# Optimization experiments

Measured on AMD Instinct MI355X. Metric: run time of the kernel, lower is better.

The kernel has to match this reference:

```python
import jax, jax.numpy as jnp
import numpy as np

B = 8; A = 9; NUM_CLASSES = 80
BRANCH_HW = [(80, 80), (40, 40)]; STRIDES = [8, 16]
IMG_H, IMG_W = 640, 640
CLASS_OFFSETS = [0, 0]
SCORE_THR = 0.05; NMS_THR = 0.5; MARGIN = 0.0
PRE_NMS = 1000; POST_NMS = 300
MIN_H, MIN_W = 0.0, 0.0
BBOX_CLIP = float(np.log(1000.0 / 16.0))  # torchvision-style dw/dh clamp


def _make_anchors(H, W, stride):
    # A square anchors per cell, grid-aligned (x1,y1,x2,y2)
    sizes = np.array([16., 32., 64., 20., 40., 80., 24., 48., 96.])[:A]
    cx = (np.arange(W) + 0.5) * stride
    cy = (np.arange(H) + 0.5) * stride
    cy_g, cx_g = np.meshgrid(cy, cx, indexing='ij')  # [H,W]
    half = sizes / 2.0  # [A]
    x1 = cx_g[..., None] - half; y1 = cy_g[..., None] - half
    x2 = cx_g[..., None] + half; y2 = cy_g[..., None] + half
    anc = np.stack([x1, y1, x2, y2], -1).astype(np.float32)  # [H,W,A,4]
    anc = anc.reshape(H, W, A * 4).transpose(2, 0, 1)  # [A*4,H,W]
    return jnp.asarray(np.broadcast_to(anc[None], (B,) + anc.shape).copy())


def setup_inputs() -> dict:
    key = jax.random.key(0)
    ks = jax.random.split(key, 2)
    out = {}
    for i, (Hh, Ww) in enumerate(BRANCH_HW):
        d = jax.random.normal(ks[i], (B, Hh, Ww, A, 4 + NUM_CLASSES), jnp.float32)
        d = d.at[..., :4].multiply(0.25)  # keep box deltas in a sane range
        out['data%d' % i] = d.reshape(B, Hh, Ww, A * (4 + NUM_CLASSES)).transpose(0, 3, 1, 2)
        out['anchors%d' % i] = _make_anchors(Hh, Ww, STRIDES[i])
    return out


def _unfold(t, d):
    b = t.shape[0]
    return jnp.transpose(t, (0, 2, 3, 1)).reshape(b, -1, d)


def _decode(deltas, anchors):
    # BoxCoder((1,1,1,1)).decode_single
    aw = anchors[..., 2] - anchors[..., 0]; ah = anchors[..., 3] - anchors[..., 1]
    acx = anchors[..., 0] + 0.5 * aw; acy = anchors[..., 1] + 0.5 * ah
    dx, dy, dw, dh = (deltas[..., 0], deltas[..., 1], deltas[..., 2], deltas[..., 3])
    pcx = dx * aw + acx; pcy = dy * ah + acy
    pw = jnp.exp(jnp.minimum(dw, BBOX_CLIP)) * aw
    ph = jnp.exp(jnp.minimum(dh, BBOX_CLIP)) * ah
    return jnp.stack([pcx - 0.5 * pw, pcy - 0.5 * ph, pcx + 0.5 * pw, pcy + 0.5 * ph], -1)


def _iou(b):
    area = (b[:, 2] - b[:, 0]) * (b[:, 3] - b[:, 1])
    lt = jnp.maximum(b[:, None, :2], b[None, :, :2])
    rb = jnp.minimum(b[:, None, 2:], b[None, :, 2:])
    wh = jnp.clip(rb - lt, 0.0)
    inter = wh[..., 0] * wh[..., 1]
    return inter / (area[:, None] + area[None, :] - inter + 1e-9)


def _nms_single(boxes, cls, scores):
    # sort by score, take pre_nms_top_k
    sc, idx = jax.lax.top_k(scores, PRE_NMS)
    b = boxes[idx]; c = cls[idx]
    # score threshold + min-hw validity filter (masked instead of dynamic slice)
    valid = (sc >= SCORE_THR) & (b[:, 0] < b[:, 2] - MIN_W) & (b[:, 1] < b[:, 3] - MIN_H)
    iou = _iou(b)  # [PRE,PRE]
    rng = jnp.arange(PRE_NMS)

    def body(i, keep):
        # box j suppressed by kept box i if IoU>thr and score_i - score_j > margin
        sup = keep[i] & (iou[i] > NMS_THR) & ((sc[i] - sc) > MARGIN) & (rng > i)
        return keep & (~sup)

    keep = jax.lax.fori_loop(0, PRE_NMS, body, valid)
    # kept boxes first (score order preserved), then pad_zero to POST_NMS
    order = jnp.argsort(jnp.where(keep, rng, rng + PRE_NMS))[:POST_NMS]
    km = keep[order]
    return (jnp.where(km[:, None], b[order], 0.0),
            jnp.where(km, sc[order], 0.0),
            jnp.where(km, c[order], 0.0))


def reference(data0, data1, anchors0, anchors1):
    datas = [data0, data1]; ancs = [anchors0, anchors1]
    fa, deltas, scores, offs = [], [], [], []
    for i in range(2):
        fa.append(_unfold(ancs[i], 4))
        u = _unfold(datas[i], 4 + NUM_CLASSES)
        deltas.append(u[..., :4]); scores.append(u[..., 4:])
        offs.append(jnp.full((1, u.shape[1]), float(CLASS_OFFSETS[i]), jnp.float32))
    fa = jnp.concatenate(fa, 1); deltas = jnp.concatenate(deltas, 1)
    scores = jnp.concatenate(scores, 1); offs = jnp.concatenate(offs, 1)
    max_sc = scores.max(-1)
    cls = jnp.argmax(scores, -1).astype(jnp.float32) + offs
    boxes = _decode(deltas, fa)
    # clip to image
    x = jnp.clip(boxes[..., 0::2], 0.0, float(IMG_W))
    y = jnp.clip(boxes[..., 1::2], 0.0, float(IMG_H))
    boxes = jnp.stack([x[..., 0], y[..., 0], x[..., 1], y[..., 1]], -1)
    return jax.vmap(_nms_single)(boxes, cls, max_sc)  # ([B,POST,4],[B,POST],[B,POST])
```

## Files before the change

### kernel.cpp

```cpp
#include <hip/hip_runtime.h>
#include <math.h>

#pragma clang fp contract(off)

#define BB      8
#define AA      9
#define NCLS    80
#define NTOT    72000
#define PRE     1000
#define POST    300
#define CAP     4096
#define BCLIP   4.135166556742356f
#define NBLK0   1440
#define NBLK1   360
#define DS1BASE 1843200

__device__ __constant__ float c_sizes[9] = {16.f,32.f,64.f,20.f,40.f,80.f,24.f,48.f,96.f};

__device__ inline unsigned fkey(float s) {
    unsigned u = __float_as_uint(s);
    return (u & 0x80000000u) ? ~u : (u | 0x80000000u);
}
__device__ inline float unfkey(unsigned u) {
    return __uint_as_float((u & 0x80000000u) ? (u ^ 0x80000000u) : ~u);
}

template<int BR>
__device__ inline void stream_impl(int bx, const float* __restrict__ data,
                                   unsigned long long* __restrict__ partial,
                                   float* __restrict__ dstage,
                                   unsigned long long* lkey)
{
    constexpr int ROWF4 = BR ? 400 : 1600;
    int slab, cg, hwq;
    if (BR == 0) { slab = bx / 20; int r = bx % 20; cg = r / 4; hwq = r % 4; }
    else         { slab = bx / 5;  cg = bx % 5;  hwq = 0; }
    int b = slab / 9, a = slab - (slab / 9) * 9;
    int nch = cg ? 16 : 20;
    int c_first = cg ? (4 + cg * 16) : 0;

    for (int i = threadIdx.x; i < 1600; i += 256) lkey[i] = 0ULL;
    __syncthreads();

    const float4* d4 = (const float4*)data;
    size_t rowbase = (size_t)(b * 756 + a * 84 + c_first) * ROWF4 + hwq * 400;
    float4* ds4 = (float4*)dstage;

    int tid = threadIdx.x;
    int rr2 = tid + 256;
    bool s2 = (rr2 < 400);

    for (int c0 = 0; c0 < nch; c0 += 4) {
        float4 v[8];
        #pragma unroll
        for (int u = 0; u < 4; u++) {
            size_t base = rowbase + (size_t)(c0 + u) * ROWF4;
            v[2 * u]     = d4[base + tid];
            v[2 * u + 1] = s2 ? d4[base + rr2] : make_float4(0.f, 0.f, 0.f, 0.f);
        }
        #pragma unroll
        for (int u = 0; u < 4; u++) {
            int ch = c_first + c0 + u;
            if (ch < 4) {
                size_t di0, di1;
                if (BR) { di0 = (size_t)(DS1BASE / 4) + (size_t)(slab * 4 + ch) * 400 + tid;
                          di1 = di0 + 256; }
                else    { di0 = (size_t)(slab * 4 + ch) * 1600 + hwq * 400 + tid;
                          di1 = di0 + 256; }
                ds4[di0] = v[2 * u];
                if (s2) ds4[di1] = v[2 * u + 1];
            } else {
                unsigned icls = ~(unsigned)(ch - 4);
                float4 x = v[2 * u];
                int cell = tid * 4;
                atomicMax(&lkey[cell + 0], ((unsigned long long)fkey(x.x) << 32) | icls);
                atomicMax(&lkey[cell + 1], ((unsigned long long)fkey(x.y) << 32) | icls);
                atomicMax(&lkey[cell + 2], ((unsigned long long)fkey(x.z) << 32) | icls);
                atomicMax(&lkey[cell + 3], ((unsigned long long)fkey(x.w) << 32) | icls);
                if (s2) {
                    float4 y = v[2 * u + 1];
                    int cell2 = rr2 * 4;
                    atomicMax(&lkey[cell2 + 0], ((unsigned long long)fkey(y.x) << 32) | icls);
                    atomicMax(&lkey[cell2 + 1], ((unsigned long long)fkey(y.y) << 32) | icls);
                    atomicMax(&lkey[cell2 + 2], ((unsigned long long)fkey(y.z) << 32) | icls);
                    atomicMax(&lkey[cell2 + 3], ((unsigned long long)fkey(y.w) << 32) | icls);
                }
            }
        }
    }
    __syncthreads();

    size_t pbase = (size_t)cg * 576000 + (size_t)b * 72000
                 + (BR ? (size_t)(57600 + a * 1600) : (size_t)(a * 6400 + hwq * 1600));
    for (int cell = threadIdx.x; cell < 1600; cell += 256)
        partial[pbase + cell] = lkey[cell];
}

__global__ __launch_bounds__(256) void k_stream(
    const float* __restrict__ data0, const float* __restrict__ data1,
    unsigned long long* __restrict__ partial, float* __restrict__ dstage)
{
    __shared__ unsigned long long lkey[1600];
    int bx = blockIdx.x;
    if (bx < NBLK0) stream_impl<0>(bx, data0, partial, dstage, lkey);
    else            stream_impl<1>(bx - NBLK0, data1, partial, dstage, lkey);
}

__global__ __launch_bounds__(256) void k_cells(
    const unsigned long long* __restrict__ partial, const float* __restrict__ dstage,
    float* __restrict__ boxes, float* __restrict__ scores, float* __restrict__ cls,
    unsigned* __restrict__ chist)
{
    __shared__ unsigned lh[256];
    int tid = threadIdx.x;
    lh[tid] = 0;
    __syncthreads();

    int b = blockIdx.y;
    int mm = blockIdx.x * 256 + tid;
    if (mm < 36000) {
        const ulonglong2* p2 = (const ulonglong2*)partial;
        ulonglong2 best = p2[(size_t)b * 36000 + mm];
        #pragma unroll
        for (int g = 1; g < 5; g++) {
            ulonglong2 v = p2[(size_t)g * 288000 + (size_t)b * 36000 + mm];
            if (v.x > best.x) best.x = v.x;
            if (v.y > best.y) best.y = v.y;
        }
        unsigned long long kk[2] = { best.x, best.y };

        int m0 = mm * 2;
        int a, hw, W, STRIDE;
        size_t dbase;
        if (m0 < 57600) {
            a = m0 / 6400; hw = m0 - a * 6400; W = 80; STRIDE = 8;
            dbase = (size_t)((b * 9 + a) * 4) * 6400 + hw;
        } else {
            int m1 = m0 - 57600;
            a = m1 / 1600; hw = m1 - a * 1600; W = 40; STRIDE = 16;
            dbase = (size_t)DS1BASE + (size_t)((b * 9 + a) * 4) * 1600 + hw;
        }
        size_t cstride = (m0 < 57600) ? 6400 : 1600;
        float2 dx = *(const float2*)(dstage + dbase);
        float2 dy = *(const float2*)(dstage + dbase + cstride);
        float2 dw = *(const float2*)(dstage + dbase + 2 * cstride);
        float2 dh = *(const float2*)(dstage + dbase + 3 * cstride);
        float dxa[2] = {dx.x, dx.y}, dya[2] = {dy.x, dy.y};
        float dwa[2] = {dw.x, dw.y}, dha[2] = {dh.x, dh.y};

        float sz = c_sizes[a];
        size_t o = (size_t)b * NTOT + m0;

        #pragma unroll
        for (int k = 0; k < 2; k++) {
            int hwk = hw + k;
            int h = hwk / W;
            int w = hwk - h * W;
            float cy = (h + 0.5f) * (float)STRIDE;
            float cx = (w + 0.5f) * (float)STRIDE;
            float pcx = dxa[k] * sz + cx;
            float pcy = dya[k] * sz + cy;
            float pw  = expf(fminf(dwa[k], BCLIP)) * sz;
            float ph  = expf(fminf(dha[k], BCLIP)) * sz;
            float x1 = fminf(fmaxf(pcx - 0.5f * pw, 0.f), 640.f);
            float y1 = fminf(fmaxf(pcy - 0.5f * ph, 0.f), 640.f);
            float x2 = fminf(fmaxf(pcx + 0.5f * pw, 0.f), 640.f);
            float y2 = fminf(fmaxf(pcy + 0.5f * ph, 0.f), 640.f);
            ((float4*)boxes)[o + k] = make_float4(x1, y1, x2, y2);
            scores[o + k] = unfkey((unsigned)(kk[k] >> 32));
            cls[o + k]    = (float)(~(unsigned)kk[k]);
            atomicAdd(&lh[(unsigned)(kk[k] >> 56)], 1u);
        }
    }
    __syncthreads();
    if (lh[tid]) atomicAdd(&chist[b * 256 + tid], lh[tid]);
}

__global__ __launch_bounds__(256) void k_cscan(const unsigned* __restrict__ chist,
                                               unsigned* __restrict__ Cca)
{
    __shared__ unsigned S[256];
    int b = blockIdx.x, tid = threadIdx.x;
    S[tid] = chist[b * 256 + tid];
    __syncthreads();
    for (int off = 1; off < 256; off <<= 1) {
        unsigned v = S[tid] + ((tid + off < 256) ? S[tid + off] : 0u);
        __syncthreads();
        S[tid] = v;
        __syncthreads();
    }
    if (S[tid] >= (unsigned)PRE && (tid == 255 || S[tid + 1] < (unsigned)PRE)) {
        Cca[b * 2]     = (unsigned)tid;
        Cca[b * 2 + 1] = (tid == 255) ? 0u : S[tid + 1];
    }
}

__global__ __launch_bounds__(256) void k_fine(const float* __restrict__ scores,
                                              const unsigned* __restrict__ Cca,
                                              unsigned* __restrict__ fhist)
{
    __shared__ unsigned lh[256];
    int tid = threadIdx.x;
    lh[tid] = 0;
    __syncthreads();
    int b = blockIdx.y;
    unsigned C = Cca[b * 2];
    int m4 = blockIdx.x * 256 + tid;
    if (m4 < NTOT / 4) {
        float sv[4];
        *(float4*)sv = ((const float4*)(scores + (size_t)b * NTOT))[m4];
        #pragma unroll
        for (int k = 0; k < 4; k++) {
            unsigned u = fkey(sv[k]);
            if ((u >> 24) == C) atomicAdd(&lh[(u >> 16) & 0xFF], 1u);
        }
    }
    __syncthreads();
    if (lh[tid]) atomicAdd(&fhist[b * 256 + tid], lh[tid]);
}

__global__ __launch_bounds__(256) void k_fthr(const unsigned* __restrict__ fhist,
                                              const unsigned* __restrict__ Cca,
                                              unsigned* __restrict__ T)
{
    __shared__ unsigned S[256];
    int b = blockIdx.x, tid = threadIdx.x;
    unsigned C = Cca[b * 2], ca = Cca[b * 2 + 1];
    S[tid] = fhist[b * 256 + tid];
    __syncthreads();
    for (int off = 1; off < 256; off <<= 1) {
        unsigned v = S[tid] + ((tid + off < 256) ? S[tid + off] : 0u);
        __syncthreads();
        S[tid] = v;
        __syncthreads();
    }
    if (ca + S[tid] >= (unsigned)PRE && (tid == 255 || ca + S[tid + 1] < (unsigned)PRE))
        T[b] = (C << 8) | (unsigned)tid;
}

__global__ __launch_bounds__(256) void k_compact(const float* __restrict__ scores,
                                                 const unsigned* __restrict__ T,
                                                 unsigned* __restrict__ cnt,
                                                 unsigned long long* __restrict__ cand)
{
    int m4 = blockIdx.x * 256 + threadIdx.x;
    int b = blockIdx.y;
    if (m4 >= NTOT / 4) return;
    float sv[4];
    *(float4*)sv = ((const float4*)(scores + (size_t)b * NTOT))[m4];
    unsigned Tb = T[b];
    #pragma unroll
    for (int k = 0; k < 4; k++) {
        unsigned u = fkey(sv[k]);
        if ((u >> 16) >= Tb) {
            int m = m4 * 4 + k;
            int n;
            if (m < 57600) { int a = m / 6400; int hw = m - a * 6400; n = hw * 9 + a; }
            else { int mm = m - 57600; int a = mm / 1600; int hw = mm - a * 1600; n = 57600 + hw * 9 + a; }
            unsigned pos = atomicAdd(&cnt[b], 1u);
            if (pos < CAP)
                cand[(size_t)b * CAP + pos] = ((unsigned long long)u << 32) | (unsigned)(~(unsigned)n);
        }
    }
}

__global__ __launch_bounds__(1024) void k_sort(
    const unsigned long long* __restrict__ cand, const unsigned* __restrict__ cnt,
    const float* __restrict__ boxes, const float* __restrict__ scores, const float* __restrict__ cls,
    float* __restrict__ sboxes, float* __restrict__ sscores, float* __restrict__ scls)
{
    __shared__ unsigned long long keys[CAP];
    int b = blockIdx.x, tid = threadIdx.x;
    int c = min((int)cnt[b], CAP);
    int P = 1024;
    while (P < c) P <<= 1;
    for (int i = tid; i < P; i += 1024)
        keys[i] = (i < c) ? cand[(size_t)b * CAP + i] : 0ULL;

    for (int k2 = 2; k2 <= P; k2 <<= 1)
        for (int j = k2 >> 1; j > 0; j >>= 1) {
            __syncthreads();
            for (int i = tid; i < P; i += 1024) {
                int l = i ^ j;
                if (l > i) {
                    unsigned long long x = keys[i], y = keys[l];
                    bool up = ((i & k2) == 0);
                    if ((x > y) == up) { keys[i] = y; keys[l] = x; }
                }
            }
        }
    __syncthreads();

    if (tid < PRE) {
        unsigned long long key = keys[P - 1 - tid];
        int n = (int)~(unsigned)(key & 0xFFFFFFFFu);
        int m;
        if (n < 57600) { int hw = n / 9; int a = n - hw * 9; m = a * 6400 + hw; }
        else { int n2 = n - 57600; int hw = n2 / 9; int a = n2 - hw * 9; m = 57600 + a * 1600 + hw; }
        size_t src = (size_t)b * NTOT + m;
        ((float4*)sboxes)[b * 1024 + tid] = ((const float4*)boxes)[src];
        sscores[b * 1024 + tid] = scores[src];
        scls[b * 1024 + tid] = cls[src];
    }
}

__global__ __launch_bounds__(1024) void k_mask(const float* __restrict__ sboxes,
                                               const float* __restrict__ sscores,
                                               unsigned long long* __restrict__ maskT)
{
    __shared__ float4 bx[64];
    __shared__ float  sl[64];
    int b = blockIdx.y, w = blockIdx.x, tid = threadIdx.x;
    if (tid < 64) {
        int i = w * 64 + tid;
        bx[tid] = ((const float4*)sboxes)[b * 1024 + i];
        sl[tid] = sscores[b * 1024 + i];
    }
    __syncthreads();
    int j = tid;
    unsigned long long* dst = &maskT[((size_t)(b * 16) + w) * 1024 + j];
    if (j >= PRE || w * 64 >= j) { *dst = 0ULL; return; }

    float4 bj = ((const float4*)sboxes)[b * 1024 + j];
    float sj = sscores[b * 1024 + j];
    float areaj = (bj.z - bj.x) * (bj.w - bj.y);
    unsigned long long bits = 0;
    int iend = min(64, j - w * 64);
    for (int ii = 0; ii < iend; ii++) {
        float4 bi = bx[ii];
        float ix1 = fmaxf(bi.x, bj.x), iy1 = fmaxf(bi.y, bj.y);
        float ix2 = fminf(bi.z, bj.z), iy2 = fminf(bi.w, bj.w);
        float iw = fmaxf(ix2 - ix1, 0.f), ih = fmaxf(iy2 - iy1, 0.f);
        float inter = iw * ih;
        float areai = (bi.z - bi.x) * (bi.w - bi.y);
        float iou = inter / (areai + areaj - inter + 1e-9f);
        if (iou > 0.5f && sl[ii] > sj) bits |= 1ull << ii;
    }
    *dst = bits;
}

__global__ __launch_bounds__(64) void k_nms(const unsigned long long* __restrict__ maskT,
                                            const float* __restrict__ sboxes,
                                            const float* __restrict__ sscores,
                                            const float* __restrict__ scls,
                                            float* __restrict__ out)
{
    int b = blockIdx.x, lane = threadIdx.x;
    const unsigned long long* base = maskT + (size_t)b * 16 * 1024;

    unsigned validbits = 0;
    #pragma unroll
    for (int c = 0; c < 16; c++) {
        int r = c * 64 + lane;
        bool v = false;
        if (r < PRE) {
            float sc = sscores[b * 1024 + r];
            float4 bbx = ((const float4*)sboxes)[b * 1024 + r];
            v = (sc >= 0.05f) && (bbx.x < bbx.z) && (bbx.y < bbx.w);
        }
        validbits |= (v ? 1u : 0u) << c;
    }

    unsigned long long keptw[16];
    #pragma unroll
    for (int c = 0; c < 16; c++) {
        unsigned long long acc = 0, col = 0;
        #pragma unroll
        for (int w = 0; w <= c; w++) {
            unsigned long long m = base[(w << 10) + c * 64 + lane];
            if (w < c) acc |= m & keptw[w];
            else       col = m;
        }
        bool alive = (((validbits >> c) & 1u) != 0u) && (acc == 0ULL);

        unsigned long long ab = __ballot(alive);
        unsigned long long kw = 0;
        while (ab) {
            int f = __ffsll((unsigned long long)ab) - 1;
            kw |= 1ULL << f;
            alive = alive && (lane != f) && (((col >> f) & 1ULL) == 0ULL);
            ab = __ballot(alive);
        }
        keptw[c] = kw;
    }

    __shared__ unsigned long long kws[16];
    __shared__ int pfx[17];
    if (lane == 0) {
        int s = 0;
        #pragma unroll
        for (int w = 0; w < 16; w++) {
            kws[w] = keptw[w];
            pfx[w] = s;
            s += __popcll(keptw[w]);
        }
        pfx[16] = s;
    }
    __syncthreads();
    int nk = pfx[16];

    float* ob = out;
    float* os = out + BB * POST * 4;
    float* oc = os + BB * POST;

    for (int r = lane; r < PRE; r += 64) {
        int w = r >> 6;
        unsigned long long kw = kws[w];
        if ((kw >> (r & 63)) & 1ULL) {
            int rank = pfx[w] + __popcll(kw & ((1ULL << (r & 63)) - 1ULL));
            if (rank < POST) {
                ((float4*)ob)[b * POST + rank] = ((const float4*)sboxes)[b * 1024 + r];
                os[b * POST + rank] = sscores[b * 1024 + r];
                oc[b * POST + rank] = scls[b * 1024 + r];
            }
        }
    }
    for (int p = nk + lane; p < POST; p += 64) {
        ((float4*)ob)[b * POST + p] = make_float4(0.f, 0.f, 0.f, 0.f);
        os[b * POST + p] = 0.f;
        oc[b * POST + p] = 0.f;
    }
}

extern "C" void kernel_launch(void* const* d_in, const int* in_sizes, int n_in,
                              void* d_out, int out_size, void* d_ws, size_t ws_size,
                              hipStream_t stream)
{
    const float* data0 = (const float*)d_in[0];
    const float* data1 = (const float*)d_in[2];
    for (int i = 0; i < n_in; i++) {
        if (in_sizes[i] == 8 * 756 * 6400) data0 = (const float*)d_in[i];
        else if (in_sizes[i] == 8 * 756 * 1600) data1 = (const float*)d_in[i];
    }

    char* ws = (char*)d_ws;
    size_t off = 0;
    auto alloc = [&](size_t bytes) -> char* {
        char* p = ws + off;
        off = (off + bytes + 255) & ~(size_t)255;
        return p;
    };

    float* boxes   = (float*)alloc((size_t)BB * NTOT * 4 * 4);
    float* scores  = (float*)alloc((size_t)BB * NTOT * 4);
    float* cls     = (float*)alloc((size_t)BB * NTOT * 4);
    unsigned* cnt   = (unsigned*)alloc(BB * 4);
    unsigned* chist = (unsigned*)alloc(BB * 256 * 4);
    unsigned* fhist = (unsigned*)alloc(BB * 256 * 4);
    unsigned* Cca  = (unsigned*)alloc(BB * 2 * 4);
    unsigned* T    = (unsigned*)alloc(BB * 4);
    unsigned long long* cand = (unsigned long long*)alloc((size_t)BB * CAP * 8);
    float* sboxes  = (float*)alloc((size_t)BB * 1024 * 4 * 4);
    float* sscores = (float*)alloc((size_t)BB * 1024 * 4);
    float* scls    = (float*)alloc((size_t)BB * 1024 * 4);
    unsigned long long* maskT = (unsigned long long*)alloc((size_t)BB * 16 * 1024 * 8);
    unsigned long long* partial = (unsigned long long*)alloc((size_t)5 * 576000 * 8);
    float* dstage  = (float*)alloc((size_t)(DS1BASE + 72 * 4 * 1600) * 4);

    (void)hipMemsetAsync(cnt, 0, 256 + 2 * (size_t)BB * 256 * 4, stream);

    k_stream<<<NBLK0 + NBLK1, 256, 0, stream>>>(data0, data1, partial, dstage);

    dim3 gc(141, BB);
    k_cells<<<gc, 256, 0, stream>>>(partial, dstage, boxes, scores, cls, chist);

    k_cscan<<<BB, 256, 0, stream>>>(chist, Cca);
    dim3 gf((NTOT / 4 + 255) / 256, BB);
    k_fine<<<gf, 256, 0, stream>>>(scores, Cca, fhist);
    k_fthr<<<BB, 256, 0, stream>>>(fhist, Cca, T);

    k_compact<<<gf, 256, 0, stream>>>(scores, T, cnt, cand);

    k_sort<<<BB, 1024, 0, stream>>>(cand, cnt, boxes, scores, cls, sboxes, sscores, scls);

    dim3 g5(16, BB);
    k_mask<<<g5, 1024, 0, stream>>>(sboxes, sscores, maskT);

    k_nms<<<BB, 64, 0, stream>>>(maskT, sboxes, sscores, scls, (float*)d_out);
}
```

Baseline: 458.0 us.

## Fuse class-max streaming with box decode and fold scan kernels into consumers

Replaces the split stream and cells kernels with one fused kernel. Each thread reads its four delta channels and loops over all 80 class channels in registers, so the partial-key buffer, the delta staging buffer and the shared-memory 64-bit atomics are gone. The coarse and fine histogram scans are recomputed redundantly inside k_fine and k_compact, which removes the k_cscan and k_fthr launches. The cost is fewer blocks (720, with only 200 of 256 threads active), each doing a longer serial channel loop, which may reduce memory-level parallelism. Every block also repeats the 256-entry scans.

```diff
diff --git a/kernel.cpp b/kernel.cpp
--- a/kernel.cpp
+++ b/kernel.cpp
@@ -11,9 +11,6 @@
 #define POST    300
 #define CAP     4096
 #define BCLIP   4.135166556742356f
-#define NBLK0   1440
-#define NBLK1   360
-#define DS1BASE 1843200
 
 __device__ __constant__ float c_sizes[9] = {16.f,32.f,64.f,20.f,40.f,80.f,24.f,48.f,96.f};
 
@@ -21,167 +18,111 @@
     unsigned u = __float_as_uint(s);
     return (u & 0x80000000u) ? ~u : (u | 0x80000000u);
 }
-__device__ inline float unfkey(unsigned u) {
-    return __uint_as_float((u & 0x80000000u) ? (u ^ 0x80000000u) : ~u);
-}
 
 template<int BR>
-__device__ inline void stream_impl(int bx, const float* __restrict__ data,
-                                   unsigned long long* __restrict__ partial,
-                                   float* __restrict__ dstage,
-                                   unsigned long long* lkey)
-{
-    constexpr int ROWF4 = BR ? 400 : 1600;
-    int slab, cg, hwq;
-    if (BR == 0) { slab = bx / 20; int r = bx % 20; cg = r / 4; hwq = r % 4; }
-    else         { slab = bx / 5;  cg = bx % 5;  hwq = 0; }
+__device__ inline void fused_impl(int bx, const float* __restrict__ data,
+    float* __restrict__ boxes, float* __restrict__ scores, float* __restrict__ cls,
+    unsigned* __restrict__ chist, unsigned* lh)
+{
+    constexpr int ROWF4  = BR ? 400 : 1600;
+    constexpr int W      = BR ? 40 : 80;
+    constexpr int STRIDE = BR ? 16 : 8;
+    constexpr int NQ     = BR ? 2 : 8;
+
+    int slab = bx / NQ;
+    int q    = bx - slab * NQ;
     int b = slab / 9, a = slab - (slab / 9) * 9;
-    int nch = cg ? 16 : 20;
-    int c_first = cg ? (4 + cg * 16) : 0;
-
-    for (int i = threadIdx.x; i < 1600; i += 256) lkey[i] = 0ULL;
-    __syncthreads();
+    int tid = threadIdx.x;
+    bool act = tid < 200;
 
     const float4* d4 = (const float4*)data;
-    size_t rowbase = (size_t)(b * 756 + a * 84 + c_first) * ROWF4 + hwq * 400;
-    float4* ds4 = (float4*)dstage;
-
-    int tid = threadIdx.x;
-    int rr2 = tid + 256;
-    bool s2 = (rr2 < 400);
-
-    for (int c0 = 0; c0 < nch; c0 += 4) {
-        float4 v[8];
-        #pragma unroll
-        for (int u = 0; u < 4; u++) {
-            size_t base = rowbase + (size_t)(c0 + u) * ROWF4;
-            v[2 * u]     = d4[base + tid];
-            v[2 * u + 1] = s2 ? d4[base + rr2] : make_float4(0.f, 0.f, 0.f, 0.f);
-        }
-        #pragma unroll
-        for (int u = 0; u < 4; u++) {
-            int ch = c_first + c0 + u;
-            if (ch < 4) {
-                size_t di0, di1;
-                if (BR) { di0 = (size_t)(DS1BASE / 4) + (size_t)(slab * 4 + ch) * 400 + tid;
-                          di1 = di0 + 256; }
-                else    { di0 = (size_t)(slab * 4 + ch) * 1600 + hwq * 400 + tid;
-                          di1 = di0 + 256; }
-                ds4[di0] = v[2 * u];
-                if (s2) ds4[di1] = v[2 * u + 1];
-            } else {
-                unsigned icls = ~(unsigned)(ch - 4);
-                float4 x = v[2 * u];
-                int cell = tid * 4;
-                atomicMax(&lkey[cell + 0], ((unsigned long long)fkey(x.x) << 32) | icls);
-                atomicMax(&lkey[cell + 1], ((unsigned long long)fkey(x.y) << 32) | icls);
-                atomicMax(&lkey[cell + 2], ((unsigned long long)fkey(x.z) << 32) | icls);
-                atomicMax(&lkey[cell + 3], ((unsigned long long)fkey(x.w) << 32) | icls);
-                if (s2) {
-                    float4 y = v[2 * u + 1];
-                    int cell2 = rr2 * 4;
-                    atomicMax(&lkey[cell2 + 0], ((unsigned long long)fkey(y.x) << 32) | icls);
-                    atomicMax(&lkey[cell2 + 1], ((unsigned long long)fkey(y.y) << 32) | icls);
-                    atomicMax(&lkey[cell2 + 2], ((unsigned long long)fkey(y.z) << 32) | icls);
-                    atomicMax(&lkey[cell2 + 3], ((unsigned long long)fkey(y.w) << 32) | icls);
-                }
+    size_t rowbase = (size_t)(b * 756 + a * 84) * ROWF4 + q * 200;
+
+    if (act) {
+        float4 del[4];
+        #pragma unroll
+        for (int u = 0; u < 4; u++)
+            del[u] = d4[rowbase + (size_t)u * ROWF4 + tid];
+
+        float best[4];
+        int   bc[4];
+        #pragma unroll
+        for (int k = 0; k < 4; k++) { best[k] = -INFINITY; bc[k] = 0; }
+
+        for (int c0 = 4; c0 < 84; c0 += 8) {
+            float4 v[8];
+            #pragma unroll
+            for (int u = 0; u < 8; u++)
+                v[u] = d4[rowbase + (size_t)(c0 + u) * ROWF4 + tid];
+            #pragma unroll
+            for (int u = 0; u < 8; u++) {
+                int c = c0 + u - 4;
+                float s0[4];
+                *(float4*)s0 = v[u];
+                #pragma unroll
+                for (int k = 0; k < 4; k++)
+                    if (s0[k] > best[k]) { best[k] = s0[k]; bc[k] = c; }
             }
         }
-    }
-    __syncthreads();
-
-    size_t pbase = (size_t)cg * 576000 + (size_t)b * 72000
-                 + (BR ? (size_t)(57600 + a * 1600) : (size_t)(a * 6400 + hwq * 1600));
-    for (int cell = threadIdx.x; cell < 1600; cell += 256)
-        partial[pbase + cell] = lkey[cell];
-}
-
-__global__ __launch_bounds__(256) void k_stream(
-    const float* __restrict__ data0, const float* __restrict__ data1,
-    unsigned long long* __restrict__ partial, float* __restrict__ dstage)
-{
-    __shared__ unsigned long long lkey[1600];
-    int bx = blockIdx.x;
-    if (bx < NBLK0) stream_impl<0>(bx, data0, partial, dstage, lkey);
-    else            stream_impl<1>(bx - NBLK0, data1, partial, dstage, lkey);
-}
-
-__global__ __launch_bounds__(256) void k_cells(
-    const unsigned long long* __restrict__ partial, const float* __restrict__ dstage,
-    float* __restrict__ boxes, float* __restrict__ scores, float* __restrict__ cls,
-    unsigned* __restrict__ chist)
-{
-    __shared__ unsigned lh[256];
-    int tid = threadIdx.x;
-    lh[tid] = 0;
-    __syncthreads();
-
-    int b = blockIdx.y;
-    int mm = blockIdx.x * 256 + tid;
-    if (mm < 36000) {
-        const ulonglong2* p2 = (const ulonglong2*)partial;
-        ulonglong2 best = p2[(size_t)b * 36000 + mm];
-        #pragma unroll
-        for (int g = 1; g < 5; g++) {
-            ulonglong2 v = p2[(size_t)g * 288000 + (size_t)b * 36000 + mm];
-            if (v.x > best.x) best.x = v.x;
-            if (v.y > best.y) best.y = v.y;
-        }
-        unsigned long long kk[2] = { best.x, best.y };
-
-        int m0 = mm * 2;
-        int a, hw, W, STRIDE;
-        size_t dbase;
-        if (m0 < 57600) {
-            a = m0 / 6400; hw = m0 - a * 6400; W = 80; STRIDE = 8;
-            dbase = (size_t)((b * 9 + a) * 4) * 6400 + hw;
-        } else {
-            int m1 = m0 - 57600;
-            a = m1 / 1600; hw = m1 - a * 1600; W = 40; STRIDE = 16;
-            dbase = (size_t)DS1BASE + (size_t)((b * 9 + a) * 4) * 1600 + hw;
-        }
-        size_t cstride = (m0 < 57600) ? 6400 : 1600;
-        float2 dx = *(const float2*)(dstage + dbase);
-        float2 dy = *(const float2*)(dstage + dbase + cstride);
-        float2 dw = *(const float2*)(dstage + dbase + 2 * cstride);
-        float2 dh = *(const float2*)(dstage + dbase + 3 * cstride);
-        float dxa[2] = {dx.x, dx.y}, dya[2] = {dy.x, dy.y};
-        float dwa[2] = {dw.x, dw.y}, dha[2] = {dh.x, dh.y};
 
         float sz = c_sizes[a];
-        size_t o = (size_t)b * NTOT + m0;
-
-        #pragma unroll
-        for (int k = 0; k < 2; k++) {
-            int hwk = hw + k;
-            int h = hwk / W;
-            int w = hwk - h * W;
+        float dx[4], dy[4], dwv[4], dhv[4];
+        *(float4*)dx  = del[0];
+        *(float4*)dy  = del[1];
+        *(float4*)dwv = del[2];
+        *(float4*)dhv = del[3];
+
+        int ml0 = q * 800 + tid * 4;
+        size_t obase = (size_t)b * NTOT + (BR ? (57600 + a * 1600) : (a * 6400));
+
+        #pragma unroll
+        for (int k = 0; k < 4; k++) {
+            int hw = ml0 + k;
+            int h = hw / W, w = hw - h * W;
             float cy = (h + 0.5f) * (float)STRIDE;
             float cx = (w + 0.5f) * (float)STRIDE;
-            float pcx = dxa[k] * sz + cx;
-            float pcy = dya[k] * sz + cy;
-            float pw  = expf(fminf(dwa[k], BCLIP)) * sz;
-            float ph  = expf(fminf(dha[k], BCLIP)) * sz;
+            float pcx = dx[k] * sz + cx;
+            float pcy = dy[k] * sz + cy;
+            float pw  = expf(fminf(dwv[k], BCLIP)) * sz;
+            float ph  = expf(fminf(dhv[k], BCLIP)) * sz;
             float x1 = fminf(fmaxf(pcx - 0.5f * pw, 0.f), 640.f);
             float y1 = fminf(fmaxf(pcy - 0.5f * ph, 0.f), 640.f);
             float x2 = fminf(fmaxf(pcx + 0.5f * pw, 0.f), 640.f);
             float y2 = fminf(fmaxf(pcy + 0.5f * ph, 0.f), 640.f);
-            ((float4*)boxes)[o + k] = make_float4(x1, y1, x2, y2);
-            scores[o + k] = unfkey((unsigned)(kk[k] >> 32));
-            cls[o + k]    = (float)(~(unsigned)kk[k]);
-            atomicAdd(&lh[(unsigned)(kk[k] >> 56)], 1u);
+            size_t o = obase + hw;
+            ((float4*)boxes)[o] = make_float4(x1, y1, x2, y2);
+            scores[o] = best[k];
+            cls[o]    = (float)bc[k];
+            atomicAdd(&lh[fkey(best[k]) >> 24], 1u);
         }
     }
     __syncthreads();
     if (lh[tid]) atomicAdd(&chist[b * 256 + tid], lh[tid]);
 }
 
-__global__ __launch_bounds__(256) void k_cscan(const unsigned* __restrict__ chist,
-                                               unsigned* __restrict__ Cca)
+__global__ __launch_bounds__(256) void k_fused(
+    const float* __restrict__ data0, const float* __restrict__ data1,
+    float* __restrict__ boxes, float* __restrict__ scores, float* __restrict__ cls,
+    unsigned* __restrict__ chist)
+{
+    __shared__ unsigned lh[256];
+    lh[threadIdx.x] = 0;
+    __syncthreads();
+    int bx = blockIdx.x;
+    if (bx < 576) fused_impl<0>(bx, data0, boxes, scores, cls, chist, lh);
+    else          fused_impl<1>(bx - 576, data1, boxes, scores, cls, chist, lh);
+}
+
+__global__ __launch_bounds__(256) void k_fine(const float* __restrict__ scores,
+                                              const unsigned* __restrict__ chist,
+                                              unsigned* __restrict__ fhist)
 {
     __shared__ unsigned S[256];
-    int b = blockIdx.x, tid = threadIdx.x;
-    S[tid] = chist[b * 256 + tid];
+    __shared__ unsigned lh[256];
+    __shared__ unsigned sC;
+    int tid = threadIdx.x, b = blockIdx.y;
+    S[tid]  = chist[b * 256 + tid];
+    lh[tid] = 0;
     __syncthreads();
     for (int off = 1; off < 256; off <<= 1) {
         unsigned v = S[tid] + ((tid + off < 256) ? S[tid + off] : 0u);
@@ -189,22 +130,10 @@
         S[tid] = v;
         __syncthreads();
     }
-    if (S[tid] >= (unsigned)PRE && (tid == 255 || S[tid + 1] < (unsigned)PRE)) {
-        Cca[b * 2]     = (unsigned)tid;
-        Cca[b * 2 + 1] = (tid == 255) ? 0u : S[tid + 1];
-    }
-}
-
-__global__ __launch_bounds__(256) void k_fine(const float* __restrict__ scores,
-                                              const unsigned* __restrict__ Cca,
-                                              unsigned* __restrict__ fhist)
-{
-    __shared__ unsigned lh[256];
-    int tid = threadIdx.x;
-    lh[tid] = 0;
-    __syncthreads();
-    int b = blockIdx.y;
-    unsigned C = Cca[b * 2];
+    if (S[tid] >= (unsigned)PRE && (tid == 255 || S[tid + 1] < (unsigned)PRE)) sC = tid;
+    __syncthreads();
+    unsigned C = sC;
+
     int m4 = blockIdx.x * 256 + tid;
     if (m4 < NTOT / 4) {
         float sv[4];
@@ -219,14 +148,17 @@
     if (lh[tid]) atomicAdd(&fhist[b * 256 + tid], lh[tid]);
 }
 
-__global__ __launch_bounds__(256) void k_fthr(const unsigned* __restrict__ fhist,
-                                              const unsigned* __restrict__ Cca,
-                                              unsigned* __restrict__ T)
+__global__ __launch_bounds__(256) void k_compact(const float* __restrict__ scores,
+                                                 const unsigned* __restrict__ chist,
+                                                 const unsigned* __restrict__ fhist,
+                                                 unsigned* __restrict__ cnt,
+                                                 unsigned long long* __restrict__ cand)
 {
     __shared__ unsigned S[256];
-    int b = blockIdx.x, tid = threadIdx.x;
-    unsigned C = Cca[b * 2], ca = Cca[b * 2 + 1];
-    S[tid] = fhist[b * 256 + tid];
+    __shared__ unsigned sC, sCa, sT;
+    int tid = threadIdx.x, b = blockIdx.y;
+
+    S[tid] = chist[b * 256 + tid];
     __syncthreads();
     for (int off = 1; off < 256; off <<= 1) {
         unsigned v = S[tid] + ((tid + off < 256) ? S[tid + off] : 0u);
@@ -234,21 +166,29 @@
         S[tid] = v;
         __syncthreads();
     }
+    if (S[tid] >= (unsigned)PRE && (tid == 255 || S[tid + 1] < (unsigned)PRE)) {
+        sC  = tid;
+        sCa = (tid == 255) ? 0u : S[tid + 1];
+    }
+    __syncthreads();
+    unsigned C = sC, ca = sCa;
+    S[tid] = fhist[b * 256 + tid];
+    __syncthreads();
+    for (int off = 1; off < 256; off <<= 1) {
+        unsigned v = S[tid] + ((tid + off < 256) ? S[tid + off] : 0u);
+        __syncthreads();
+        S[tid] = v;
+        __syncthreads();
+    }
     if (ca + S[tid] >= (unsigned)PRE && (tid == 255 || ca + S[tid + 1] < (unsigned)PRE))
-        T[b] = (C << 8) | (unsigned)tid;
-}
-
-__global__ __launch_bounds__(256) void k_compact(const float* __restrict__ scores,
-                                                 const unsigned* __restrict__ T,
-                                                 unsigned* __restrict__ cnt,
-                                                 unsigned long long* __restrict__ cand)
-{
-    int m4 = blockIdx.x * 256 + threadIdx.x;
-    int b = blockIdx.y;
+        sT = (C << 8) | (unsigned)tid;
+    __syncthreads();
+    unsigned Tb = sT;
+
+    int m4 = blockIdx.x * 256 + tid;
     if (m4 >= NTOT / 4) return;
     float sv[4];
     *(float4*)sv = ((const float4*)(scores + (size_t)b * NTOT))[m4];
-    unsigned Tb = T[b];
     #pragma unroll
     for (int k = 0; k < 4; k++) {
         unsigned u = fkey(sv[k]);
@@ -447,29 +387,20 @@
     unsigned* cnt   = (unsigned*)alloc(BB * 4);
     unsigned* chist = (unsigned*)alloc(BB * 256 * 4);
     unsigned* fhist = (unsigned*)alloc(BB * 256 * 4);
-    unsigned* Cca  = (unsigned*)alloc(BB * 2 * 4);
-    unsigned* T    = (unsigned*)alloc(BB * 4);
     unsigned long long* cand = (unsigned long long*)alloc((size_t)BB * CAP * 8);
     float* sboxes  = (float*)alloc((size_t)BB * 1024 * 4 * 4);
     float* sscores = (float*)alloc((size_t)BB * 1024 * 4);
     float* scls    = (float*)alloc((size_t)BB * 1024 * 4);
     unsigned long long* maskT = (unsigned long long*)alloc((size_t)BB * 16 * 1024 * 8);
-    unsigned long long* partial = (unsigned long long*)alloc((size_t)5 * 576000 * 8);
-    float* dstage  = (float*)alloc((size_t)(DS1BASE + 72 * 4 * 1600) * 4);
 
     (void)hipMemsetAsync(cnt, 0, 256 + 2 * (size_t)BB * 256 * 4, stream);
 
-    k_stream<<<NBLK0 + NBLK1, 256, 0, stream>>>(data0, data1, partial, dstage);
-
-    dim3 gc(141, BB);
-    k_cells<<<gc, 256, 0, stream>>>(partial, dstage, boxes, scores, cls, chist);
-
-    k_cscan<<<BB, 256, 0, stream>>>(chist, Cca);
+    k_fused<<<720, 256, 0, stream>>>(data0, data1, boxes, scores, cls, chist);
+
     dim3 gf((NTOT / 4 + 255) / 256, BB);
-    k_fine<<<gf, 256, 0, stream>>>(scores, Cca, fhist);
-    k_fthr<<<BB, 256, 0, stream>>>(fhist, Cca, T);
-
-    k_compact<<<gf, 256, 0, stream>>>(scores, T, cnt, cand);
+    k_fine<<<gf, 256, 0, stream>>>(scores, chist, fhist);
+
+    k_compact<<<gf, 256, 0, stream>>>(scores, chist, fhist, cnt, cand);
 
     k_sort<<<BB, 1024, 0, stream>>>(cand, cnt, boxes, scores, cls, sboxes, sscores, scls);
 
```

Result: faster. 438.6 us (-4.2%).
